# Kernel optimization log

Hardware: AMD Instinct MI355X
Metric: run time of the kernel (lower is better)

The kernel has to match this reference:

```python
import jax, jax.numpy as jnp
import numpy as np

D_MODEL, D_HIDDEN, N_EXPERTS = 1024, 4096, 8
CAP_FACTOR, LBL_COEF, ZLOSS_COEF = 1.25, 0.01, 0.0


def setup_inputs() -> dict:
    key = jax.random.key(0)
    ks = jax.random.split(key, 4)
    B, T = 4, 2048
    x = jax.random.normal(ks[0], (B, T, D_MODEL), dtype=jnp.float32)
    # router linear
    Wr = jax.random.normal(ks[1], (D_MODEL, N_EXPERTS), jnp.float32) / np.sqrt(D_MODEL).astype(np.float32)
    br = jnp.zeros((N_EXPERTS,), jnp.float32)
    # per-expert MLP: fc1 [D->H], gelu, fc2 [H->D]
    W1 = jax.random.normal(ks[2], (N_EXPERTS, D_MODEL, D_HIDDEN), jnp.float32) / np.sqrt(D_MODEL).astype(np.float32)
    b1 = jnp.zeros((N_EXPERTS, D_HIDDEN), jnp.float32)
    W2 = jax.random.normal(ks[3], (N_EXPERTS, D_HIDDEN, D_MODEL), jnp.float32) / np.sqrt(D_HIDDEN).astype(np.float32)
    b2 = jnp.zeros((N_EXPERTS, D_MODEL), jnp.float32)
    return {"x": x, "Wr": Wr, "br": br, "W1": W1, "b1": b1, "W2": W2, "b2": b2}


def reference(x, Wr, br, W1, b1, W2, b2):
    B, T, D = x.shape
    N = B * T
    E = Wr.shape[1]
    cap = int(CAP_FACTOR * (N / E) + 1)  # static Python int

    h = x.reshape(N, D)
    # --- Top1Router ---
    logits = h @ Wr + br                              # [N, E]
    probs = jax.nn.softmax(logits, axis=-1)
    top1 = jnp.argmax(probs, axis=-1)                 # [N]
    w = jnp.take_along_axis(probs, top1[:, None], axis=1)  # [N, 1]
    assign = jax.nn.one_hot(top1, E, dtype=jnp.float32)    # constant wrt grads
    importance = probs.mean(axis=0)
    load = jax.lax.stop_gradient(assign).mean(axis=0)
    lb_loss = E * jnp.sum(importance * load)
    z_loss = jnp.mean(jax.nn.logsumexp(logits, axis=-1) ** 2)

    # --- capacity-based dispatch (first `cap` tokens per expert, token order) ---
    pos = (jnp.cumsum(assign, axis=0) * assign).sum(axis=-1).astype(jnp.int32) - 1  # [N] slot within expert
    keep = pos < cap
    slot = jnp.where(keep, pos, cap)  # dropped tokens -> overflow slot `cap`
    xe = jnp.zeros((E, cap + 1, D), x.dtype).at[top1, slot].set(h)[:, :cap]  # [E, cap, D]

    # --- per-expert MLP as grouped GEMMs ---
    he = jax.nn.gelu(jnp.einsum('ecd,edh->ech', xe, W1) + b1[:, None, :])    # [E, cap, H]
    ye = jnp.einsum('ech,ehd->ecd', he, W2) + b2[:, None, :]                 # [E, cap, D]

    # --- combine (gather back, scale by router weight, zero dropped) ---
    out = ye[top1, jnp.minimum(pos, cap - 1)] * w   # [N, D]
    out = jnp.where(keep[:, None], out, jnp.zeros((), x.dtype))
    y = out.reshape(B, T, D)
    aux = LBL_COEF * lb_loss + ZLOSS_COEF * z_loss
    return (y, aux)
```

## Files before the change

kernel.cpp:

```cpp
#include <hip/hip_runtime.h>
#include <hip/hip_bf16.h>

#define N_TOK 8192
#define DM    1024
#define DH    4096
#define NE    8
#define CAP   1281
#define CAPR  1408
#define ISTR  1536

typedef unsigned short u16;
typedef __attribute__((ext_vector_type(8))) __bf16 bf16x8;
typedef __attribute__((ext_vector_type(8))) short short8;
typedef __attribute__((ext_vector_type(4))) short s16x4;
typedef __attribute__((ext_vector_type(4))) float f4;

__device__ __forceinline__ u16 f2bf(float f){
  union { float f; unsigned u; } v; v.f = f;
  unsigned r = v.u + 0x7fffu + ((v.u >> 16) & 1u);
  return (u16)(r >> 16);
}

__device__ __forceinline__ float gelu_fast(float v){
  float u = 0.7978845608028654f * (v + 0.044715f * v * v * v);
  return v * __builtin_amdgcn_rcpf(1.0f + __expf(-2.0f * u));
}

__device__ __forceinline__ void gl2lds16(const void* g, void* l){
  __builtin_amdgcn_global_load_lds((const __attribute__((address_space(1))) void*)g,
                                   (__attribute__((address_space(3))) void*)l, 16, 0, 0);
}

__device__ __forceinline__ void tcvt_tile(const float* __restrict__ ip, u16* __restrict__ op,
                                          int K, int Nn, int n0, int k0, int tt, float* tile){
  int kr = tt>>4, nc = (tt&15)*4;
  #pragma unroll
  for (int ii=0;ii<4;ii++){
    f4 v = *(const f4*)&ip[(size_t)(k0+kr+16*ii)*Nn + n0 + nc];
    float* row = &tile[(kr+16*ii)*65 + nc];
    row[0]=v[0]; row[1]=v[1]; row[2]=v[2]; row[3]=v[3];
  }
  __syncthreads();
  int nr = tt>>2, kc = (tt&3)*16;
  short8 o0, o1;
  #pragma unroll
  for (int c=0;c<8;c++){
    o0[c] = (short)f2bf(tile[(kc+c)*65 + nr]);
    o1[c] = (short)f2bf(tile[(kc+8+c)*65 + nr]);
  }
  *(short8*)&op[(size_t)(n0+nr)*K + k0 + kc] = o0;
  *(short8*)&op[(size_t)(n0+nr)*K + k0 + kc + 8] = o1;
}

__global__ __launch_bounds__(256) void tcvt1_k(const float* __restrict__ W1, u16* __restrict__ W1T){
  __shared__ float tile[64*65];
  int local = blockIdx.x;
  int bx = local & 63, by = (local >> 6) & 15, bz = local >> 10;
  size_t mb = (size_t)bz * (size_t)DM * (size_t)DH;
  tcvt_tile(W1 + mb, W1T + mb, DM, DH, bx*64, by*64, threadIdx.x, tile);
}

__global__ __launch_bounds__(256) void router_k(const float* __restrict__ x, const float* __restrict__ Wr,
    const float* __restrict__ br, u16* __restrict__ Xb, int* __restrict__ top1,
    float* __restrict__ wgt, float* __restrict__ impSum){
  __shared__ float pSh[4][8];
  int wid = threadIdx.x >> 6, lane = threadIdx.x & 63;
  int n = blockIdx.x * 4 + wid;
  const float* xr = x + (size_t)n * DM;
  u16* xbr = Xb + (size_t)n * DM;
  float acc[8];
  #pragma unroll
  for (int e=0;e<8;e++) acc[e]=0.f;
  #pragma unroll
  for (int c=0;c<4;c++){
    int d0 = c*256 + lane*4;
    f4 xv = *(const f4*)(xr + d0);
    s16x4 xb;
    #pragma unroll
    for (int j=0;j<4;j++) xb[j] = (short)f2bf(xv[j]);
    *(s16x4*)(xbr + d0) = xb;
    #pragma unroll
    for (int j=0;j<4;j++){
      const float* wrow = Wr + (size_t)(d0+j)*NE;
      float xs = xv[j];
      #pragma unroll
      for (int e=0;e<8;e++) acc[e] = fmaf(xs, wrow[e], acc[e]);
    }
  }
  #pragma unroll
  for (int off=32; off>0; off>>=1){
    #pragma unroll
    for (int e=0;e<8;e++) acc[e] += __shfl_down(acc[e], off, 64);
  }
  if (lane==0){
    float lg[8]; float mx = -1e30f;
    #pragma unroll
    for (int e=0;e<8;e++){ lg[e] = acc[e] + br[e]; mx = fmaxf(mx, lg[e]); }
    float p[8], s=0.f;
    #pragma unroll
    for (int e=0;e<8;e++){ p[e] = expf(lg[e]-mx); s += p[e]; }
    int bt=0; float bv=lg[0];
    #pragma unroll
    for (int e=1;e<8;e++){ if (lg[e]>bv){ bv=lg[e]; bt=e; } }
    float inv = 1.f/s;
    top1[n] = bt; wgt[n] = p[bt]*inv;
    #pragma unroll
    for (int e=0;e<8;e++) pSh[wid][e] = p[e]*inv;
  }
  __syncthreads();
  if (threadIdx.x < 8){
    int e = threadIdx.x;
    atomicAdd(&impSum[e], pSh[0][e]+pSh[1][e]+pSh[2][e]+pSh[3][e]);
  }
}

__global__ __launch_bounds__(1024) void scan_k(const int* __restrict__ top1, int* __restrict__ idx,
    int* __restrict__ cnt, int* __restrict__ dropList, int* __restrict__ nDrop,
    const float* __restrict__ impSum, float* __restrict__ auxOut){
  __shared__ int waveCnt[16][8];
  __shared__ int wavePre[16][8];
  __shared__ int chunkTot[8];
  __shared__ int base_s[8];
  int tid = threadIdx.x, wid = tid>>6, lane = tid&63;
  if (tid < 8) base_s[tid] = 0;
  __syncthreads();
  for (int c=0;c<8;c++){
    int t = c*1024 + tid;
    int e = top1[t];
    int myPre = 0;
    #pragma unroll
    for (int ex=0; ex<8; ex++){
      unsigned long long mk = __ballot(e == ex);
      if (lane == 0) waveCnt[wid][ex] = __popcll(mk);
      if (ex == e) myPre = __popcll(mk & ((1ull<<lane)-1ull));
    }
    __syncthreads();
    if (tid < 8){
      int run = 0;
      for (int wv=0; wv<16; wv++){ wavePre[wv][tid] = run; run += waveCnt[wv][tid]; }
      chunkTot[tid] = run;
    }
    __syncthreads();
    int pos = base_s[e] + wavePre[wid][e] + myPre;
    if (pos < CAP) idx[e*ISTR + pos] = t;
    else { int d = atomicAdd(nDrop, 1); dropList[d] = t; }
    __syncthreads();
    if (tid < 8) base_s[tid] += chunkTot[tid];
    __syncthreads();
  }
  if (tid < 8){
    cnt[tid] = base_s[tid] < CAP ? base_s[tid] : CAP;
  }
  if (tid == 0){
    float s = 0.f;
    for (int e=0;e<8;e++) s += (impSum[e]*(1.f/N_TOK)) * ((float)base_s[e]*(1.f/N_TOK));
    *auxOut = 0.01f * 8.f * s;
  }
}

__global__ __launch_bounds__(256) void zdrop_k(const int* __restrict__ dropList,
    const int* __restrict__ nDrop, float* __restrict__ y){
  int nd = *nDrop;
  for (int i = blockIdx.x; i < nd; i += gridDim.x){
    int t = dropList[i];
    f4* row = (f4*)(y + (size_t)t * DM);
    f4 z; z[0]=0.f; z[1]=0.f; z[2]=0.f; z[3]=0.f;
    row[threadIdx.x] = z;
  }
}

#define LDA(buf, m, kk) (*(const bf16x8*)&lds[(buf)*16384 + (aBase ^ ((kk)*32)) + (m)*1024])
#define LDB(buf, n, kk) (*(const bf16x8*)&lds[32768 + (buf)*16384 + (bBase ^ ((kk)*32)) + (n)*1024])

#define SA_J(buf, j, kc) gl2lds16(aS[j] + (size_t)(kc)*64, &lds[(buf)*16384 + ((j)*512 + t)*8])
#define SB_ALLM(buf, kc) do{ \
  gl2lds16(bS[0] + (size_t)(kc)*64, &lds[32768 + (buf)*16384 + (0*512 + t)*8]); \
  gl2lds16(bS[1] + (size_t)(kc)*64, &lds[32768 + (buf)*16384 + (1*512 + t)*8]); \
  gl2lds16(bS[2] + (size_t)(kc)*64, &lds[32768 + (buf)*16384 + (2*512 + t)*8]); \
  gl2lds16(bS[3] + (size_t)(kc)*64, &lds[32768 + (buf)*16384 + (3*512 + t)*8]); }while(0)

#define SB0 __builtin_amdgcn_sched_barrier(0)
#define LGKM(n) do{ asm volatile("s_waitcnt lgkmcnt(" #n ")" ::: "memory"); SB0; }while(0)

#define READ_A(dst, mbase, buf) do{ \
  dst[0][0]=LDA(buf,(mbase),0);   dst[0][1]=LDA(buf,(mbase),1); \
  dst[1][0]=LDA(buf,(mbase)+1,0); dst[1][1]=LDA(buf,(mbase)+1,1); }while(0)

#define MFMA_PAIR(q, A_) \
  _Pragma("unroll") for (int j_=0;j_<2;j_++) \
    _Pragma("unroll") for (int n_=0;n_<4;n_++) \
      _Pragma("unroll") for (int kk_=0;kk_<2;kk_++) \
        acc[2*(q)+j_][n_] = __builtin_amdgcn_mfma_f32_16x16x32_bf16(A_[j_][kk_], Bf[n_][kk_], acc[2*(q)+j_][n_], 0,0,0);

#define KTILE(buf, ktv, NTv) do{ \
  int kc1 = (ktv)+1 < (NTv) ? (ktv)+1 : (NTv)-1; \
  int kc2 = (ktv)+2 < (NTv) ? (ktv)+2 : (NTv)-1; \
  asm volatile("s_waitcnt vmcnt(6)" ::: "memory"); \
  __builtin_amdgcn_s_barrier(); \
  SA_J((buf)^1, 1, kc1); SA_J((buf)^1, 3, kc1); \
  _Pragma("unroll") for (int n_=0;n_<4;n_++){ Bf[n_][0] = LDB(buf,n_,0); Bf[n_][1] = LDB(buf,n_,1); } \
  READ_A(aA, 0, buf); \
  SB0; \
  READ_A(aB, 2, buf); \
  LGKM(4); \
  __builtin_amdgcn_s_setprio(1); MFMA_PAIR(0, aA); __builtin_amdgcn_s_setprio(0); \
  __builtin_amdgcn_s_barrier(); \
  SB_ALLM(buf, kc2); \
  READ_A(aA, 4, buf); \
  LGKM(4); \
  __builtin_amdgcn_s_setprio(1); MFMA_PAIR(1, aB); __builtin_amdgcn_s_setprio(0); \
  __builtin_amdgcn_s_barrier(); \
  SA_J(buf, 0, kc2); SA_J(buf, 2, kc2); \
  READ_A(aB, 6, buf); \
  LGKM(4); \
  __builtin_amdgcn_s_setprio(1); MFMA_PAIR(2, aA); __builtin_amdgcn_s_setprio(0); \
  __builtin_amdgcn_s_barrier(); \
  LGKM(0); \
  __builtin_amdgcn_s_setprio(1); MFMA_PAIR(3, aB); __builtin_amdgcn_s_setprio(0); \
}while(0)

#define GEMM_PROLOGUE() do{ \
  SB_ALLM(0, 0); \
  SA_J(0,0,0); SA_J(0,2,0); \
  SA_J(0,1,0); SA_J(0,3,0); \
  SB_ALLM(1, 1); \
  SA_J(1,0,1); SA_J(1,2,1); }while(0)

__global__ __launch_bounds__(512, 2) void gemm1_k(
    const u16* __restrict__ Xb, const u16* __restrict__ W1T,
    const float* __restrict__ b1, const int* __restrict__ idx,
    const int* __restrict__ cnt, u16* __restrict__ He,
    const float* __restrict__ W2, u16* __restrict__ W2T)
{
  __shared__ __align__(16) u16 lds[65536];
  int bid = blockIdx.x;
  int t = threadIdx.x;
  if (bid >= 768){
    int half = t >> 8, tt = t & 255;
    int tau = (bid - 768)*2 + half;
    int bx = tau & 15, by = (tau >> 4) & 63, bz = tau >> 10;
    size_t mb = (size_t)bz * (size_t)DH * (size_t)DM;
    float* tile = ((float*)lds) + half*4160;
    tcvt_tile(W2 + mb, W2T + mb, DH, DM, bx*64, by*64, tt, tile);
    return;
  }
  int x = bid & 7, k = bid >> 3;
  int g = x*16 + k/6;
  int ntS = k - (k/6)*6;
  int e = g >> 4, mtH = g & 15;
  int cn = cnt[e];
  if (ntS*256 >= cn) return;
  int lane = t&63, wid = t>>6;
  int waveM = wid>>2, waveN = wid&3;
  int rA = lane&15, kb = lane>>4, s = rA&7;

  const u16* aS[4]; const u16* bS[4];
  #pragma unroll
  for (int j=0;j<4;j++){
    int pos = j*512 + t;
    int row = pos>>3, ch = pos&7;
    int gcb = ch ^ (row&7);
    aS[j] = W1T + ((size_t)e*DH + mtH*256 + row)*DM + gcb*8;
    int slotrow = ntS*256 + row;
    int token = (slotrow < cn) ? idx[e*ISTR + slotrow] : 0;
    bS[j] = Xb + (size_t)token*DM + gcb*8;
  }
  f4 acc[8][4];
  #pragma unroll
  for (int m=0;m<8;m++)
    #pragma unroll
    for (int n=0;n<4;n++)
      #pragma unroll
      for (int j=0;j<4;j++) acc[m][n][j]=0.f;

  int aBase = (waveM*128 + rA)*64 + (kb ^ s)*8;
  int bBase = (waveN*64  + rA)*64 + (kb ^ s)*8;
  bf16x8 Bf[4][2], aA[2][2], aB[2][2];

  GEMM_PROLOGUE();
  const int NT = DM/64;
  #pragma unroll 1
  for (int i=0;i<NT/2;i++){
    KTILE(0, 2*i,   NT);
    KTILE(1, 2*i+1, NT);
  }
  asm volatile("s_waitcnt vmcnt(0) lgkmcnt(0)" ::: "memory");

  int rG = lane>>4;
  #pragma unroll
  for (int m=0;m<8;m++){
    int h0 = mtH*256 + waveM*128 + m*16 + rG*4;
    f4 b4 = *(const f4*)&b1[e*DH + h0];
    #pragma unroll
    for (int n=0;n<4;n++){
      int slot = ntS*256 + waveN*64 + n*16 + rA;
      if (slot < cn){
        s16x4 v;
        #pragma unroll
        for (int j=0;j<4;j++) v[j] = (short)f2bf(gelu_fast(acc[m][n][j] + b4[j]));
        *(s16x4*)&He[((size_t)e*CAPR + slot)*DH + h0] = v;
      }
    }
  }
}

__global__ __launch_bounds__(512, 2) void gemm2_k(
    const u16* __restrict__ He, const u16* __restrict__ W2T,
    const float* __restrict__ b2, const int* __restrict__ idx,
    const int* __restrict__ cnt, const float* __restrict__ wgt,
    float* __restrict__ y)
{
  int bid = blockIdx.x;
  int x = bid & 7, k = bid >> 3;
  int g = x*4 + k/6;
  int mt = k - (k/6)*6;
  int e = g >> 2, nt = g & 3;
  int cn = cnt[e];
  if (mt*256 >= cn) return;
  __shared__ __align__(16) u16 lds[65536];
  int t = threadIdx.x, lane = t&63, wid = t>>6;
  int waveM = wid>>2, waveN = wid&3;
  int rA = lane&15, kb = lane>>4, s = rA&7;

  const u16* aS[4]; const u16* bS[4];
  #pragma unroll
  for (int j=0;j<4;j++){
    int pos = j*512 + t;
    int row = pos>>3, ch = pos&7;
    int gcb = ch ^ (row&7);
    int srow = mt*256 + row; if (srow >= cn) srow = cn-1;
    aS[j] = He  + ((size_t)e*CAPR + srow)*DH + gcb*8;
    bS[j] = W2T + ((size_t)e*DM + nt*256 + row)*DH + gcb*8;
  }
  f4 acc[8][4];
  #pragma unroll
  for (int m=0;m<8;m++)
    #pragma unroll
    for (int n=0;n<4;n++)
      #pragma unroll
      for (int j=0;j<4;j++) acc[m][n][j]=0.f;

  int aBase = (waveM*128 + rA)*64 + (kb ^ s)*8;
  int bBase = (waveN*64  + rA)*64 + (kb ^ s)*8;
  bf16x8 Bf[4][2], aA[2][2], aB[2][2];

  GEMM_PROLOGUE();
  const int NT = DH/64;
  #pragma unroll 1
  for (int i=0;i<NT/2;i++){
    KTILE(0, 2*i,   NT);
    KTILE(1, 2*i+1, NT);
  }
  asm volatile("s_waitcnt vmcnt(0) lgkmcnt(0)" ::: "memory");

  int rG = lane>>4;
  float bias_[4];
  #pragma unroll
  for (int n=0;n<4;n++) bias_[n] = b2[e*DM + nt*256 + waveN*64 + n*16 + rA];
  #pragma unroll
  for (int m=0;m<8;m++){
    int slot0 = mt*256 + waveM*128 + m*16 + rG*4;
    #pragma unroll
    for (int j=0;j<4;j++){
      int slot = slot0 + j;
      bool valid = slot < cn;
      int tk = valid ? idx[e*ISTR + slot] : 0;
      float wv = valid ? wgt[tk] : 0.f;
      float* yr = y + (size_t)tk*DM;
      #pragma unroll
      for (int n=0;n<4;n++){
        int col = nt*256 + waveN*64 + n*16 + rA;
        if (valid) yr[col] = (acc[m][n][j] + bias_[n]) * wv;
      }
    }
  }
}

extern "C" void kernel_launch(void* const* d_in, const int* in_sizes, int n_in,
                              void* d_out, int out_size, void* d_ws, size_t ws_size,
                              hipStream_t stream){
  const float* x  = (const float*)d_in[0];
  const float* Wr = (const float*)d_in[1];
  const float* br = (const float*)d_in[2];
  const float* W1 = (const float*)d_in[3];
  const float* b1 = (const float*)d_in[4];
  const float* W2 = (const float*)d_in[5];
  const float* b2 = (const float*)d_in[6];
  float* y = (float*)d_out;

  char* ws = (char*)d_ws;
  u16* Xb  = (u16*)(ws);
  u16* W1T = (u16*)(ws + 16777216ull);
  u16* W2T = (u16*)(ws + 16777216ull + 67108864ull);
  u16* He  = (u16*)(ws + 16777216ull + 2ull*67108864ull);
  char* tail = ws + 16777216ull + 2ull*67108864ull + (size_t)NE*CAPR*DH*2ull;
  int*   top1   = (int*)(tail);
  float* wgt    = (float*)(tail + 32768);
  int*   idx    = (int*)(tail + 65536);
  int*   drop   = (int*)(tail + 65536 + 49152);
  float* impSum = (float*)(tail + 65536 + 49152 + 32768);
  int*   nDrop  = (int*)((char*)impSum + 32);
  int*   cnt    = nDrop + 1;

  (void)hipMemsetAsync(impSum, 0, 64, stream);

  tcvt1_k<<<8192, 256, 0, stream>>>(W1, W1T);
  router_k<<<2048, 256, 0, stream>>>(x, Wr, br, Xb, top1, wgt, impSum);
  scan_k<<<1, 1024, 0, stream>>>(top1, idx, cnt, drop, nDrop, impSum,
                                 y + (size_t)N_TOK*DM);
  zdrop_k<<<64, 256, 0, stream>>>(drop, nDrop, y);
  gemm1_k<<<768 + 4096, 512, 0, stream>>>(Xb, W1T, b1, idx, cnt, He, W2, W2T);
  gemm2_k<<<192, 512, 0, stream>>>(He, W2T, b2, idx, cnt, wgt, y);

  (void)in_sizes; (void)n_in; (void)out_size; (void)ws_size;
}
```

Baseline: 339.8 us.

## Merge router with W1 transpose kernel and fold drop-zeroing into scan

Fuses the W1 bf16 transpose/convert blocks into the router launch as extra blocks, replaces global importance atomics with per-block partials reduced in the scan kernel, and moves drop-list handling into LDS so the scan kernel zeroes dropped rows itself. This removes a memset and two kernel launches plus their serialization gaps. The trade-off is that the single-block scan now does the partial-sum reduction and the drop zeroing serially, which could lengthen the critical path.

After: 329.8 us (median of 2 runs). -3.0%, faster.

```diff
diff --git a/kernel.cpp b/kernel.cpp
--- a/kernel.cpp
+++ b/kernel.cpp
@@ -52,20 +52,22 @@
   *(short8*)&op[(size_t)(n0+nr)*K + k0 + kc + 8] = o1;
 }
 
-__global__ __launch_bounds__(256) void tcvt1_k(const float* __restrict__ W1, u16* __restrict__ W1T){
-  __shared__ float tile[64*65];
-  int local = blockIdx.x;
-  int bx = local & 63, by = (local >> 6) & 15, bz = local >> 10;
-  size_t mb = (size_t)bz * (size_t)DM * (size_t)DH;
-  tcvt_tile(W1 + mb, W1T + mb, DM, DH, bx*64, by*64, threadIdx.x, tile);
-}
-
-__global__ __launch_bounds__(256) void router_k(const float* __restrict__ x, const float* __restrict__ Wr,
+__global__ __launch_bounds__(256) void rt_k(const float* __restrict__ x, const float* __restrict__ Wr,
     const float* __restrict__ br, u16* __restrict__ Xb, int* __restrict__ top1,
-    float* __restrict__ wgt, float* __restrict__ impSum){
-  __shared__ float pSh[4][8];
+    float* __restrict__ wgt, float* __restrict__ pPart,
+    const float* __restrict__ W1, u16* __restrict__ W1T){
+  __shared__ float shbuf[64*65];
+  int bid = blockIdx.x;
+  if (bid >= 2048){
+    int local = bid - 2048;
+    int bx = local & 63, by = (local >> 6) & 15, bz = local >> 10;
+    size_t mb = (size_t)bz * (size_t)DM * (size_t)DH;
+    tcvt_tile(W1 + mb, W1T + mb, DM, DH, bx*64, by*64, threadIdx.x, shbuf);
+    return;
+  }
+  float (*pSh)[8] = (float(*)[8])shbuf;
   int wid = threadIdx.x >> 6, lane = threadIdx.x & 63;
-  int n = blockIdx.x * 4 + wid;
+  int n = bid * 4 + wid;
   const float* xr = x + (size_t)n * DM;
   u16* xbr = Xb + (size_t)n * DM;
   float acc[8];
@@ -110,19 +112,23 @@
   __syncthreads();
   if (threadIdx.x < 8){
     int e = threadIdx.x;
-    atomicAdd(&impSum[e], pSh[0][e]+pSh[1][e]+pSh[2][e]+pSh[3][e]);
+    pPart[bid*8 + e] = pSh[0][e]+pSh[1][e]+pSh[2][e]+pSh[3][e];
   }
 }
 
 __global__ __launch_bounds__(1024) void scan_k(const int* __restrict__ top1, int* __restrict__ idx,
-    int* __restrict__ cnt, int* __restrict__ dropList, int* __restrict__ nDrop,
-    const float* __restrict__ impSum, float* __restrict__ auxOut){
+    int* __restrict__ cnt, const float* __restrict__ pPart,
+    float* __restrict__ y, float* __restrict__ auxOut){
   __shared__ int waveCnt[16][8];
   __shared__ int wavePre[16][8];
   __shared__ int chunkTot[8];
   __shared__ int base_s[8];
+  __shared__ int dropLds[6912];
+  __shared__ int nDropSh;
+  __shared__ float impLds[8];
   int tid = threadIdx.x, wid = tid>>6, lane = tid&63;
-  if (tid < 8) base_s[tid] = 0;
+  if (tid < 8){ base_s[tid] = 0; impLds[tid] = 0.f; }
+  if (tid == 0) nDropSh = 0;
   __syncthreads();
   for (int c=0;c<8;c++){
     int t = c*1024 + tid;
@@ -143,29 +149,31 @@
     __syncthreads();
     int pos = base_s[e] + wavePre[wid][e] + myPre;
     if (pos < CAP) idx[e*ISTR + pos] = t;
-    else { int d = atomicAdd(nDrop, 1); dropList[d] = t; }
+    else { int d = atomicAdd(&nDropSh, 1); dropLds[d] = t; }
     __syncthreads();
     if (tid < 8) base_s[tid] += chunkTot[tid];
     __syncthreads();
   }
-  if (tid < 8){
-    cnt[tid] = base_s[tid] < CAP ? base_s[tid] : CAP;
-  }
+  if (tid < 8) cnt[tid] = base_s[tid] < CAP ? base_s[tid] : CAP;
+  {
+    int e = tid & 7, bg = tid >> 3;
+    float ps = 0.f;
+    for (int b = bg; b < 2048; b += 128) ps += pPart[b*8 + e];
+    atomicAdd(&impLds[e], ps);
+  }
+  __syncthreads();
   if (tid == 0){
     float s = 0.f;
-    for (int e=0;e<8;e++) s += (impSum[e]*(1.f/N_TOK)) * ((float)base_s[e]*(1.f/N_TOK));
+    for (int e=0;e<8;e++) s += (impLds[e]*(1.f/N_TOK)) * ((float)base_s[e]*(1.f/N_TOK));
     *auxOut = 0.01f * 8.f * s;
   }
-}
-
-__global__ __launch_bounds__(256) void zdrop_k(const int* __restrict__ dropList,
-    const int* __restrict__ nDrop, float* __restrict__ y){
-  int nd = *nDrop;
-  for (int i = blockIdx.x; i < nd; i += gridDim.x){
-    int t = dropList[i];
-    f4* row = (f4*)(y + (size_t)t * DM);
-    f4 z; z[0]=0.f; z[1]=0.f; z[2]=0.f; z[3]=0.f;
-    row[threadIdx.x] = z;
+  int nd = nDropSh;
+  for (int i=0; i<nd; i++){
+    int t = dropLds[i];
+    if (tid < 256){
+      f4 z; z[0]=0.f; z[1]=0.f; z[2]=0.f; z[3]=0.f;
+      *(f4*)&y[(size_t)t*DM + tid*4] = z;
+    }
   }
 }
 
@@ -397,18 +405,11 @@
   int*   top1   = (int*)(tail);
   float* wgt    = (float*)(tail + 32768);
   int*   idx    = (int*)(tail + 65536);
-  int*   drop   = (int*)(tail + 65536 + 49152);
-  float* impSum = (float*)(tail + 65536 + 49152 + 32768);
-  int*   nDrop  = (int*)((char*)impSum + 32);
-  int*   cnt    = nDrop + 1;
-
-  (void)hipMemsetAsync(impSum, 0, 64, stream);
-
-  tcvt1_k<<<8192, 256, 0, stream>>>(W1, W1T);
-  router_k<<<2048, 256, 0, stream>>>(x, Wr, br, Xb, top1, wgt, impSum);
-  scan_k<<<1, 1024, 0, stream>>>(top1, idx, cnt, drop, nDrop, impSum,
-                                 y + (size_t)N_TOK*DM);
-  zdrop_k<<<64, 256, 0, stream>>>(drop, nDrop, y);
+  float* pPart  = (float*)(tail + 65536 + 49152);
+  int*   cnt    = (int*)(tail + 65536 + 49152 + 65536);
+
+  rt_k<<<2048 + 8192, 256, 0, stream>>>(x, Wr, br, Xb, top1, wgt, pPart, W1, W1T);
+  scan_k<<<1, 1024, 0, stream>>>(top1, idx, cnt, pPart, y, y + (size_t)N_TOK*DM);
   gemm1_k<<<768 + 4096, 512, 0, stream>>>(Xb, W1T, b1, idx, cnt, He, W2, W2T);
   gemm2_k<<<192, 512, 0, stream>>>(He, W2T, b2, idx, cnt, wgt, y);
 
```
